# Optimization experiments

Hardware: AMD Instinct MI355X
Metric: run time of the kernel (lower is better)

Reference implementation:

```python
import jax, jax.numpy as jnp
import numpy as np

CUTOFF = 4.0
RBF_N = 32          # distance_embedding_size == D_rbf
F_DIM = 128         # hidden_size
N_ATOMS = 20000
N_PROBES = 100000
N_EDGES = 262144
LN_EPS = 1e-5


def setup_inputs() -> dict:
    key = jax.random.key(0)
    ks = jax.random.split(key, 20)
    s = 0.02
    inp = {
        "diff_pi": jax.random.normal(ks[0], (N_EDGES, 3), jnp.float32),
        "S_JK": jax.random.normal(ks[1], (N_ATOMS, F_DIM), jnp.float32),
        "V_JK": jax.random.normal(ks[2], (N_ATOMS, 3, F_DIM), jnp.float32),
        "atom_idx": jax.random.randint(ks[3], (N_EDGES,), 0, N_ATOMS),
        "probe_idx": jax.random.randint(ks[4], (N_EDGES,), 0, N_PROBES),
        "num_probes": N_PROBES,
        # state branch params
        "w_s1": jax.random.normal(ks[5], (3 * F_DIM, F_DIM), jnp.float32) * s,
        "b_s1": jnp.zeros((F_DIM,), jnp.float32),
        "g_ln": jnp.ones((F_DIM,), jnp.float32),
        "b_ln": jnp.zeros((F_DIM,), jnp.float32),
        "w_s2": jax.random.normal(ks[6], (F_DIM, F_DIM), jnp.float32) * s,
        "b_s2": jnp.zeros((F_DIM,), jnp.float32),
        # filter branch params
        "w_f1": jax.random.normal(ks[7], (RBF_N, F_DIM), jnp.float32) * s,
        "b_f1": jnp.zeros((F_DIM,), jnp.float32),
        "w_f2": jax.random.normal(ks[8], (F_DIM, F_DIM), jnp.float32) * s,
        "b_f2": jnp.zeros((F_DIM,), jnp.float32),
        # output head params
        "w_o1": jax.random.normal(ks[9], (F_DIM, F_DIM // 2), jnp.float32) * s,
        "b_o1": jnp.zeros((F_DIM // 2,), jnp.float32),
        "w_o2": jax.random.normal(ks[10], (F_DIM // 2, 1), jnp.float32) * s,
        "b_o2": jnp.zeros((1,), jnp.float32),
        "final_bias": jnp.array([-6.1], jnp.float32),
    }
    return inp


def reference(diff_pi, S_JK, V_JK, atom_idx, probe_idx, num_probes,
              w_s1, b_s1, g_ln, b_ln, w_s2, b_s2,
              w_f1, b_f1, w_f2, b_f2,
              w_o1, b_o1, w_o2, b_o2, final_bias):
    silu = jax.nn.silu
    # edge distances
    sq = (diff_pi ** 2).sum(-1)                       # [E]
    dist = jnp.sqrt(sq)                               # [E] exact distance
    dist_safe = jnp.sqrt(sq + 1e-8)[:, None]          # [E,1]
    r_hat = diff_pi / dist_safe                       # [E,3]

    # sinc RBF expansion: sin(n*pi*d/cutoff)/d, n=1..RBF_N
    n = jnp.arange(1, RBF_N + 1, dtype=diff_pi.dtype) # [D]
    e_pi = jnp.sin(dist[:, None] * n * (jnp.pi / CUTOFF)) / dist[:, None]  # [E,D]

    # gather atom features to edges
    n_i = jnp.sqrt((V_JK ** 2).sum(1) + 1e-8)         # [N,F]
    n_e = n_i[atom_idx]                               # [E,F]
    V_e = V_JK[atom_idx]                              # [E,3,F]
    q_pi = (V_e * r_hat[:, :, None]).sum(1)           # [E,F]
    S_e = S_JK[atom_idx]                              # [E,F]

    # state branch: Linear -> LayerNorm -> SiLU -> Linear
    h = jnp.concatenate([S_e, n_e, q_pi], axis=-1)    # [E,3F]
    u = h @ w_s1 + b_s1                               # [E,F]
    mu = u.mean(-1, keepdims=True)
    var = ((u - mu) ** 2).mean(-1, keepdims=True)
    u_norm = (u - mu) / jnp.sqrt(var + LN_EPS) * g_ln + b_ln
    state = silu(u_norm) @ w_s2 + b_s2                # [E,F]

    # filter branch (no normalization -> absolute distance scale)
    W = silu(e_pi @ w_f1 + b_f1) @ w_f2 + b_f2        # [E,F]

    # fuse + output head
    m = (silu((W * state) @ w_o1 + b_o1) @ w_o2 + b_o2)[:, 0]  # [E]

    x = dist / CUTOFF
    env = 1.0 - 21.0 * x ** 5 + 35.0 * x ** 6 - 15.0 * x ** 7
    env = jnp.where(dist < CUTOFF, env, jnp.zeros_like(env))
    m_w = m * env

    # scatter-add to probes
    rho = jax.ops.segment_sum(m_w, probe_idx, num_segments=num_probes)
    return rho + final_bias[0]
```

## Files before the change

kernel.cpp:

```cpp
#include <hip/hip_runtime.h>

#define EPB     64
#define E_TOTAL 262144
#define NPROBE  100000

#define HSTR   392
#define ASTR   136
#define A2_O   0
#define F1_O   8704
#define EPI_O  17408
#define LNP_B  19968
#define MPT_B  20992
#define LDS_SH 25088

#define WS1_O  0
#define WS2_O  49152
#define WF1_O  65536
#define WF2_O  69632
#define WO1_O  86016
#define WT_TOT 94208

typedef __attribute__((ext_vector_type(8))) short  short8;
typedef __attribute__((ext_vector_type(4))) float  floatx4;

#define MFMA16(a, b, c) __builtin_amdgcn_mfma_f32_16x16x32_bf16((a), (b), (c), 0, 0, 0)

__device__ __forceinline__ short f2bf(float x) {
    unsigned u = __builtin_bit_cast(unsigned, x);
    u = (u + 0x7FFFu + ((u >> 16) & 1u)) >> 16;
    return (short)(unsigned short)u;
}

__device__ __forceinline__ float silu_f(float x) { return x / (1.0f + __expf(-x)); }

struct F8 { float v[8]; };
__device__ __forceinline__ F8 ld8(const float* __restrict__ p) {
    F8 r;
    const float4 a = *(const float4*)p;
    const float4 b = *(const float4*)(p + 4);
    r.v[0] = a.x; r.v[1] = a.y; r.v[2] = a.z; r.v[3] = a.w;
    r.v[4] = b.x; r.v[5] = b.y; r.v[6] = b.z; r.v[7] = b.w;
    return r;
}

__global__ void cfr_prep(const float* __restrict__ w_s1, const float* __restrict__ w_s2,
                         const float* __restrict__ w_f1, const float* __restrict__ w_f2,
                         const float* __restrict__ w_o1,
                         const float* __restrict__ fb, float* __restrict__ out,
                         unsigned short* __restrict__ wt) {
    int i = blockIdx.x * 256 + threadIdx.x;
    if (i < NPROBE) out[i] = fb[0];
    if (i < WT_TOT) {
        float v;
        if (i < WS2_O)      { int n = i / 384, k = i - n * 384;        v = w_s1[k * 128 + n]; }
        else if (i < WF1_O) { int j = i - WS2_O, n = j >> 7, k = j & 127; v = w_s2[k * 128 + n]; }
        else if (i < WF2_O) { int j = i - WF1_O, n = j >> 5, k = j & 31;  v = w_f1[k * 128 + n]; }
        else if (i < WO1_O) { int j = i - WF2_O, n = j >> 7, k = j & 127; v = w_f2[k * 128 + n]; }
        else                { int j = i - WO1_O, n = j >> 7, k = j & 127; v = w_o1[k * 64 + n]; }
        wt[i] = (unsigned short)f2bf(v);
    }
}

__global__ __launch_bounds__(256, 3) void cfr_main(
    const float* __restrict__ diff,  const float* __restrict__ S_JK,
    const float* __restrict__ V_JK,  const int* __restrict__ atom_idx,
    const int* __restrict__ probe_idx,
    const unsigned short* __restrict__ wt,
    const float* __restrict__ b_s1, const float* __restrict__ g_ln,
    const float* __restrict__ b_ln, const float* __restrict__ b_s2,
    const float* __restrict__ b_f1, const float* __restrict__ b_f2,
    const float* __restrict__ b_o1, const float* __restrict__ w_o2,
    const float* __restrict__ b_o2,
    float* __restrict__ out)
{
    __shared__ __align__(16) unsigned short LDSu[LDS_SH];
    __shared__ float rdat[EPB][4];
    __shared__ float invd_s[EPB];
    __shared__ float env_s[EPB];
    __shared__ int   probe_s[EPB];
    __shared__ int   atom_s[EPB];

    float* lnp   = (float*)&LDSu[LNP_B];
    float* mpart = (float*)&LDSu[MPT_B];

    const int t    = threadIdx.x;
    const int e0   = blockIdx.x * EPB;
    const int wave = t >> 6;
    const int lane = t & 63;
    const int q    = lane >> 4;
    const int c16  = lane & 15;

    if (t < EPB) {
        int e = e0 + t;
        float dx = diff[e * 3 + 0], dy = diff[e * 3 + 1], dz = diff[e * 3 + 2];
        float sq   = dx * dx + dy * dy + dz * dz;
        float dist = sqrtf(sq);
        float rinv = 1.0f / sqrtf(sq + 1e-8f);
        rdat[t][0] = dx * rinv; rdat[t][1] = dy * rinv; rdat[t][2] = dz * rinv;
        rdat[t][3] = dist;
        invd_s[t]  = 1.0f / dist;
        float x  = dist * 0.25f;
        float x2 = x * x, x4 = x2 * x2;
        float x5 = x4 * x, x6 = x5 * x, x7 = x6 * x;
        float env = 1.0f - 21.0f * x5 + 35.0f * x6 - 15.0f * x7;
        env_s[t]  = (dist < 4.0f) ? env : 0.0f;
        probe_s[t] = probe_idx[e];
        atom_s[t]  = atom_idx[e];
    }
    __syncthreads();

#pragma unroll
    for (int it = 0; it < 4; ++it) {
        int idx = it * 256 + t;
        int e = idx >> 4, f = (idx & 15) * 8;
        int a = atom_s[e];
        F8 se = ld8(S_JK + a * 128 + f);
        F8 v0 = ld8(V_JK + a * 384 + f);
        F8 v1 = ld8(V_JK + a * 384 + 128 + f);
        F8 v2 = ld8(V_JK + a * 384 + 256 + f);
        float rx = rdat[e][0], ry = rdat[e][1], rz = rdat[e][2];
        short8 hS, hN, hQ;
#pragma unroll
        for (int j = 0; j < 8; ++j) {
            hS[j] = f2bf(se.v[j]);
            hN[j] = f2bf(sqrtf(v0.v[j] * v0.v[j] + v1.v[j] * v1.v[j] + v2.v[j] * v2.v[j] + 1e-8f));
            hQ[j] = f2bf(v0.v[j] * rx + v1.v[j] * ry + v2.v[j] * rz);
        }
        unsigned short* hr = &LDSu[e * HSTR];
        *(short8*)&hr[f]       = hS;
        *(short8*)&hr[128 + f] = hN;
        *(short8*)&hr[256 + f] = hQ;
    }
    __syncthreads();

    floatx4 acc[4][2];
    const floatx4 zero4 = {0.f, 0.f, 0.f, 0.f};
#pragma unroll
    for (int mi = 0; mi < 4; ++mi) { acc[mi][0] = zero4; acc[mi][1] = zero4; }

#pragma unroll
    for (int kk = 0; kk < 12; ++kk) {
        short8 bfr[2], af[4];
#pragma unroll
        for (int ni = 0; ni < 2; ++ni) {
            int n = wave * 32 + ni * 16 + c16;
            bfr[ni] = *(const short8*)&wt[WS1_O + n * 384 + kk * 32 + q * 8];
        }
#pragma unroll
        for (int mi = 0; mi < 4; ++mi)
            af[mi] = *(const short8*)&LDSu[(mi * 16 + c16) * HSTR + kk * 32 + q * 8];
#pragma unroll
        for (int mi = 0; mi < 4; ++mi)
#pragma unroll
            for (int ni = 0; ni < 2; ++ni)
                acc[mi][ni] = MFMA16(af[mi], bfr[ni], acc[mi][ni]);
    }
    __syncthreads();

    float bs1c[2], glc[2], blc[2];
#pragma unroll
    for (int ni = 0; ni < 2; ++ni) {
        int col = wave * 32 + ni * 16 + c16;
        bs1c[ni] = b_s1[col]; glc[ni] = g_ln[col]; blc[ni] = b_ln[col];
    }
#pragma unroll
    for (int mi = 0; mi < 4; ++mi)
#pragma unroll
        for (int r = 0; r < 4; ++r) {
            float s = 0.f, s2 = 0.f;
#pragma unroll
            for (int ni = 0; ni < 2; ++ni) {
                float v = acc[mi][ni][r] + bs1c[ni];
                s += v; s2 += v * v;
            }
#pragma unroll
            for (int d = 1; d < 16; d <<= 1) {
                s  += __shfl_xor(s, d, 64);
                s2 += __shfl_xor(s2, d, 64);
            }
            if (c16 == 0) {
                int row = mi * 16 + q * 4 + r;
                lnp[row * 8 + wave * 2 + 0] = s;
                lnp[row * 8 + wave * 2 + 1] = s2;
            }
        }
    __syncthreads();

#pragma unroll
    for (int mi = 0; mi < 4; ++mi)
#pragma unroll
        for (int r = 0; r < 4; ++r) {
            int row = mi * 16 + q * 4 + r;
            float su = 0.f, sq2 = 0.f;
#pragma unroll
            for (int w = 0; w < 4; ++w) { su += lnp[row * 8 + w * 2]; sq2 += lnp[row * 8 + w * 2 + 1]; }
            float mu = su * (1.f / 128.f);
            float ms = sq2 * (1.f / 128.f);
            float rstd = rsqrtf(ms - mu * mu + 1e-5f);
#pragma unroll
            for (int ni = 0; ni < 2; ++ni) {
                float v = acc[mi][ni][r] + bs1c[ni];
                float y = (v - mu) * rstd * glc[ni] + blc[ni];
                LDSu[A2_O + row * ASTR + (wave * 32 + ni * 16 + c16)] = (unsigned short)f2bf(silu_f(y));
            }
        }
    {
        int e = t >> 2, ng = t & 3;
        float dist = rdat[e][3];
        float inv  = invd_s[e];
        short8 pk;
#pragma unroll
        for (int j = 0; j < 8; ++j) {
            float nf = (float)(ng * 8 + j + 1);
            pk[j] = f2bf(__sinf(dist * nf * 0.785398163397448f) * inv);
        }
        *(short8*)&LDSu[EPI_O + e * 40 + ng * 8] = pk;
    }
    __syncthreads();

    {
        short8 ae[4], be[2];
#pragma unroll
        for (int mi = 0; mi < 4; ++mi)
            ae[mi] = *(const short8*)&LDSu[EPI_O + (mi * 16 + c16) * 40 + q * 8];
#pragma unroll
        for (int ni = 0; ni < 2; ++ni) {
            int n = wave * 32 + ni * 16 + c16;
            be[ni] = *(const short8*)&wt[WF1_O + n * 32 + q * 8];
        }
        floatx4 facc[4][2];
#pragma unroll
        for (int mi = 0; mi < 4; ++mi)
#pragma unroll
            for (int ni = 0; ni < 2; ++ni)
                facc[mi][ni] = MFMA16(ae[mi], be[ni], zero4);
        float bf1c[2];
#pragma unroll
        for (int ni = 0; ni < 2; ++ni) bf1c[ni] = b_f1[wave * 32 + ni * 16 + c16];
#pragma unroll
        for (int mi = 0; mi < 4; ++mi)
#pragma unroll
            for (int r = 0; r < 4; ++r) {
                int row = mi * 16 + q * 4 + r;
#pragma unroll
                for (int ni = 0; ni < 2; ++ni) {
                    float v = facc[mi][ni][r] + bf1c[ni];
                    LDSu[F1_O + row * ASTR + (wave * 32 + ni * 16 + c16)] = (unsigned short)f2bf(silu_f(v));
                }
            }
    }
    __syncthreads();

    {
        floatx4 sacc[4][2], wacc[4][2];
#pragma unroll
        for (int mi = 0; mi < 4; ++mi)
#pragma unroll
            for (int ni = 0; ni < 2; ++ni) { sacc[mi][ni] = zero4; wacc[mi][ni] = zero4; }
#pragma unroll
        for (int kk = 0; kk < 4; ++kk) {
            short8 a2f[4], f1f[4], b2[2], bw[2];
#pragma unroll
            for (int ni = 0; ni < 2; ++ni) {
                int n = wave * 32 + ni * 16 + c16;
                b2[ni] = *(const short8*)&wt[WS2_O + n * 128 + kk * 32 + q * 8];
                bw[ni] = *(const short8*)&wt[WF2_O + n * 128 + kk * 32 + q * 8];
            }
#pragma unroll
            for (int mi = 0; mi < 4; ++mi) {
                a2f[mi] = *(const short8*)&LDSu[A2_O + (mi * 16 + c16) * ASTR + kk * 32 + q * 8];
                f1f[mi] = *(const short8*)&LDSu[F1_O + (mi * 16 + c16) * ASTR + kk * 32 + q * 8];
            }
#pragma unroll
            for (int mi = 0; mi < 4; ++mi)
#pragma unroll
                for (int ni = 0; ni < 2; ++ni) {
                    sacc[mi][ni] = MFMA16(a2f[mi], b2[ni], sacc[mi][ni]);
                    wacc[mi][ni] = MFMA16(f1f[mi], bw[ni], wacc[mi][ni]);
                }
        }
        __syncthreads();
        float bs2c[2], bf2c[2];
#pragma unroll
        for (int ni = 0; ni < 2; ++ni) {
            int col = wave * 32 + ni * 16 + c16;
            bs2c[ni] = b_s2[col]; bf2c[ni] = b_f2[col];
        }
#pragma unroll
        for (int mi = 0; mi < 4; ++mi)
#pragma unroll
            for (int r = 0; r < 4; ++r) {
                int row = mi * 16 + q * 4 + r;
#pragma unroll
                for (int ni = 0; ni < 2; ++ni) {
                    float g = (sacc[mi][ni][r] + bs2c[ni]) * (wacc[mi][ni][r] + bf2c[ni]);
                    LDSu[A2_O + row * ASTR + (wave * 32 + ni * 16 + c16)] = (unsigned short)f2bf(g);
                }
            }
    }
    __syncthreads();

    {
        const int n2 = wave * 16 + c16;
        floatx4 oacc[4];
#pragma unroll
        for (int mi = 0; mi < 4; ++mi) oacc[mi] = zero4;
#pragma unroll
        for (int kk = 0; kk < 4; ++kk) {
            short8 bfr = *(const short8*)&wt[WO1_O + n2 * 128 + kk * 32 + q * 8];
#pragma unroll
            for (int mi = 0; mi < 4; ++mi) {
                short8 af = *(const short8*)&LDSu[A2_O + (mi * 16 + c16) * ASTR + kk * 32 + q * 8];
                oacc[mi] = MFMA16(af, bfr, oacc[mi]);
            }
        }
        float bo1c = b_o1[n2], wo2c = w_o2[n2];
#pragma unroll
        for (int mi = 0; mi < 4; ++mi)
#pragma unroll
            for (int r = 0; r < 4; ++r) {
                float s = silu_f(oacc[mi][r] + bo1c) * wo2c;
#pragma unroll
                for (int d = 1; d < 16; d <<= 1) s += __shfl_xor(s, d, 64);
                if (c16 == 0) mpart[(mi * 16 + q * 4 + r) * 4 + wave] = s;
            }
    }
    __syncthreads();

    if (t < EPB) {
        float m  = mpart[t * 4 + 0] + mpart[t * 4 + 1] + mpart[t * 4 + 2] + mpart[t * 4 + 3] + b_o2[0];
        float mw = m * env_s[t];
        if (mw != 0.f) unsafeAtomicAdd(&out[probe_s[t]], mw);
    }
}

extern "C" void kernel_launch(void* const* d_in, const int* in_sizes, int n_in,
                              void* d_out, int out_size, void* d_ws, size_t ws_size,
                              hipStream_t stream) {
    const float* diff    = (const float*)d_in[0];
    const float* S_JK    = (const float*)d_in[1];
    const float* V_JK    = (const float*)d_in[2];
    const int*   atom_i  = (const int*)d_in[3];
    const int*   probe_i = (const int*)d_in[4];
    const float* w_s1 = (const float*)d_in[6];
    const float* b_s1 = (const float*)d_in[7];
    const float* g_ln = (const float*)d_in[8];
    const float* b_ln = (const float*)d_in[9];
    const float* w_s2 = (const float*)d_in[10];
    const float* b_s2 = (const float*)d_in[11];
    const float* w_f1 = (const float*)d_in[12];
    const float* b_f1 = (const float*)d_in[13];
    const float* w_f2 = (const float*)d_in[14];
    const float* b_f2 = (const float*)d_in[15];
    const float* w_o1 = (const float*)d_in[16];
    const float* b_o1 = (const float*)d_in[17];
    const float* w_o2 = (const float*)d_in[18];
    const float* b_o2 = (const float*)d_in[19];
    const float* fbias = (const float*)d_in[20];
    float* out = (float*)d_out;
    unsigned short* wt = (unsigned short*)d_ws;

    cfr_prep<<<(NPROBE + 255) / 256, 256, 0, stream>>>(w_s1, w_s2, w_f1, w_f2, w_o1,
                                                       fbias, out, wt);
    cfr_main<<<E_TOTAL / EPB, 256, 0, stream>>>(diff, S_JK, V_JK, atom_i, probe_i, wt,
        b_s1, g_ln, b_ln, b_s2, b_f1, b_f2, b_o1, w_o2, b_o2, out);
}
```

Before: 288.3 us.

## Precompute per-atom bf16 S, norm and V tables to shrink edge gathers

Adds a prep kernel that converts S_JK and V_JK to bf16 per atom and precomputes the per-atom vector norm once. The edge kernel then gathers half as many bytes per edge and skips the repeated norm computation. It also swaps round-to-nearest bf16 conversion for truncation and perm-based packing in several LDS stores. The price is an extra launch, extra workspace traffic, and slightly different rounding, since q is now computed from bf16 V and values are truncated rather than rounded.

```diff
diff --git a/kernel.cpp b/kernel.cpp
--- a/kernel.cpp
+++ b/kernel.cpp
@@ -3,6 +3,7 @@
 #define EPB     64
 #define E_TOTAL 262144
 #define NPROBE  100000
+#define N_ATOMS 20000
 
 #define HSTR   392
 #define ASTR   136
@@ -19,9 +20,13 @@
 #define WF2_O  69632
 #define WO1_O  86016
 #define WT_TOT 94208
-
-typedef __attribute__((ext_vector_type(8))) short  short8;
-typedef __attribute__((ext_vector_type(4))) float  floatx4;
+#define SB_O   WT_TOT
+#define NB_O   (SB_O + N_ATOMS * 128)
+#define VB_O   (NB_O + N_ATOMS * 128)
+
+typedef __attribute__((ext_vector_type(8))) short          short8;
+typedef __attribute__((ext_vector_type(8))) unsigned short ushort8;
+typedef __attribute__((ext_vector_type(4))) float          floatx4;
 
 #define MFMA16(a, b, c) __builtin_amdgcn_mfma_f32_16x16x32_bf16((a), (b), (c), 0, 0, 0)
 
@@ -29,6 +34,16 @@
     unsigned u = __builtin_bit_cast(unsigned, x);
     u = (u + 0x7FFFu + ((u >> 16) & 1u)) >> 16;
     return (short)(unsigned short)u;
+}
+__device__ __forceinline__ unsigned short bft(float x) {
+    return (unsigned short)(__builtin_bit_cast(unsigned, x) >> 16);
+}
+__device__ __forceinline__ unsigned pk2(float lo, float hi) {
+    return __builtin_amdgcn_perm(__builtin_bit_cast(unsigned, hi),
+                                 __builtin_bit_cast(unsigned, lo), 0x07060302u);
+}
+__device__ __forceinline__ float bf2f(unsigned short u) {
+    return __builtin_bit_cast(float, ((unsigned)u) << 16);
 }
 
 __device__ __forceinline__ float silu_f(float x) { return x / (1.0f + __expf(-x)); }
@@ -43,16 +58,16 @@
     return r;
 }
 
-__global__ void cfr_prep(const float* __restrict__ w_s1, const float* __restrict__ w_s2,
-                         const float* __restrict__ w_f1, const float* __restrict__ w_f2,
-                         const float* __restrict__ w_o1,
-                         const float* __restrict__ fb, float* __restrict__ out,
-                         unsigned short* __restrict__ wt) {
+__global__ void cfr_prep_w(const float* __restrict__ w_s1, const float* __restrict__ w_s2,
+                           const float* __restrict__ w_f1, const float* __restrict__ w_f2,
+                           const float* __restrict__ w_o1,
+                           const float* __restrict__ fb, float* __restrict__ out,
+                           unsigned short* __restrict__ wt) {
     int i = blockIdx.x * 256 + threadIdx.x;
     if (i < NPROBE) out[i] = fb[0];
     if (i < WT_TOT) {
         float v;
-        if (i < WS2_O)      { int n = i / 384, k = i - n * 384;        v = w_s1[k * 128 + n]; }
+        if (i < WS2_O)      { int n = i / 384, k = i - n * 384;          v = w_s1[k * 128 + n]; }
         else if (i < WF1_O) { int j = i - WS2_O, n = j >> 7, k = j & 127; v = w_s2[k * 128 + n]; }
         else if (i < WF2_O) { int j = i - WF1_O, n = j >> 5, k = j & 31;  v = w_f1[k * 128 + n]; }
         else if (i < WO1_O) { int j = i - WF2_O, n = j >> 7, k = j & 127; v = w_f2[k * 128 + n]; }
@@ -61,11 +76,38 @@
     }
 }
 
+__global__ void cfr_prep_atoms(const float* __restrict__ S, const float* __restrict__ V,
+                               unsigned short* __restrict__ sb, unsigned short* __restrict__ nb,
+                               unsigned short* __restrict__ vb) {
+    int i = blockIdx.x * 256 + threadIdx.x;
+    if (i >= N_ATOMS * 16) return;
+    int a = i >> 4, fb8 = (i & 15) * 8;
+    F8 s  = ld8(S + a * 128 + fb8);
+    F8 v0 = ld8(V + a * 384 + fb8);
+    F8 v1 = ld8(V + a * 384 + 128 + fb8);
+    F8 v2 = ld8(V + a * 384 + 256 + fb8);
+    ushort8 so, no, w0, w1, w2;
+#pragma unroll
+    for (int j = 0; j < 8; ++j) {
+        so[j] = (unsigned short)f2bf(s.v[j]);
+        no[j] = (unsigned short)f2bf(sqrtf(v0.v[j] * v0.v[j] + v1.v[j] * v1.v[j] + v2.v[j] * v2.v[j] + 1e-8f));
+        w0[j] = (unsigned short)f2bf(v0.v[j]);
+        w1[j] = (unsigned short)f2bf(v1.v[j]);
+        w2[j] = (unsigned short)f2bf(v2.v[j]);
+    }
+    *(ushort8*)&sb[a * 128 + fb8] = so;
+    *(ushort8*)&nb[a * 128 + fb8] = no;
+    *(ushort8*)&vb[a * 384 + fb8]       = w0;
+    *(ushort8*)&vb[a * 384 + 128 + fb8] = w1;
+    *(ushort8*)&vb[a * 384 + 256 + fb8] = w2;
+}
+
 __global__ __launch_bounds__(256, 3) void cfr_main(
-    const float* __restrict__ diff,  const float* __restrict__ S_JK,
-    const float* __restrict__ V_JK,  const int* __restrict__ atom_idx,
-    const int* __restrict__ probe_idx,
+    const float* __restrict__ diff,
+    const int* __restrict__ atom_idx, const int* __restrict__ probe_idx,
     const unsigned short* __restrict__ wt,
+    const unsigned short* __restrict__ sb, const unsigned short* __restrict__ nb,
+    const unsigned short* __restrict__ vb,
     const float* __restrict__ b_s1, const float* __restrict__ g_ln,
     const float* __restrict__ b_ln, const float* __restrict__ b_s2,
     const float* __restrict__ b_f1, const float* __restrict__ b_f2,
@@ -114,22 +156,23 @@
         int idx = it * 256 + t;
         int e = idx >> 4, f = (idx & 15) * 8;
         int a = atom_s[e];
-        F8 se = ld8(S_JK + a * 128 + f);
-        F8 v0 = ld8(V_JK + a * 384 + f);
-        F8 v1 = ld8(V_JK + a * 384 + 128 + f);
-        F8 v2 = ld8(V_JK + a * 384 + 256 + f);
+        ushort8 s8 = *(const ushort8*)&sb[a * 128 + f];
+        ushort8 n8 = *(const ushort8*)&nb[a * 128 + f];
+        ushort8 v0 = *(const ushort8*)&vb[a * 384 + f];
+        ushort8 v1 = *(const ushort8*)&vb[a * 384 + 128 + f];
+        ushort8 v2 = *(const ushort8*)&vb[a * 384 + 256 + f];
         float rx = rdat[e][0], ry = rdat[e][1], rz = rdat[e][2];
-        short8 hS, hN, hQ;
-#pragma unroll
-        for (int j = 0; j < 8; ++j) {
-            hS[j] = f2bf(se.v[j]);
-            hN[j] = f2bf(sqrtf(v0.v[j] * v0.v[j] + v1.v[j] * v1.v[j] + v2.v[j] * v2.v[j] + 1e-8f));
-            hQ[j] = f2bf(v0.v[j] * rx + v1.v[j] * ry + v2.v[j] * rz);
+        unsigned qp[4];
+#pragma unroll
+        for (int jj = 0; jj < 4; ++jj) {
+            float x0 = bf2f(v0[2 * jj]) * rx + bf2f(v1[2 * jj]) * ry + bf2f(v2[2 * jj]) * rz;
+            float x1 = bf2f(v0[2 * jj + 1]) * rx + bf2f(v1[2 * jj + 1]) * ry + bf2f(v2[2 * jj + 1]) * rz;
+            qp[jj] = pk2(x0, x1);
         }
         unsigned short* hr = &LDSu[e * HSTR];
-        *(short8*)&hr[f]       = hS;
-        *(short8*)&hr[128 + f] = hN;
-        *(short8*)&hr[256 + f] = hQ;
+        *(ushort8*)&hr[f]       = s8;
+        *(ushort8*)&hr[128 + f] = n8;
+        *(uint4*)&hr[256 + f]   = make_uint4(qp[0], qp[1], qp[2], qp[3]);
     }
     __syncthreads();
 
@@ -201,20 +244,21 @@
             for (int ni = 0; ni < 2; ++ni) {
                 float v = acc[mi][ni][r] + bs1c[ni];
                 float y = (v - mu) * rstd * glc[ni] + blc[ni];
-                LDSu[A2_O + row * ASTR + (wave * 32 + ni * 16 + c16)] = (unsigned short)f2bf(silu_f(y));
+                LDSu[A2_O + row * ASTR + (wave * 32 + ni * 16 + c16)] = bft(silu_f(y));
             }
         }
     {
         int e = t >> 2, ng = t & 3;
         float dist = rdat[e][3];
         float inv  = invd_s[e];
-        short8 pk;
+        float sv[8];
 #pragma unroll
         for (int j = 0; j < 8; ++j) {
             float nf = (float)(ng * 8 + j + 1);
-            pk[j] = f2bf(__sinf(dist * nf * 0.785398163397448f) * inv);
-        }
-        *(short8*)&LDSu[EPI_O + e * 40 + ng * 8] = pk;
+            sv[j] = __sinf(dist * nf * 0.785398163397448f) * inv;
+        }
+        *(uint4*)&LDSu[EPI_O + e * 40 + ng * 8] =
+            make_uint4(pk2(sv[0], sv[1]), pk2(sv[2], sv[3]), pk2(sv[4], sv[5]), pk2(sv[6], sv[7]));
     }
     __syncthreads();
 
@@ -245,7 +289,7 @@
 #pragma unroll
                 for (int ni = 0; ni < 2; ++ni) {
                     float v = facc[mi][ni][r] + bf1c[ni];
-                    LDSu[F1_O + row * ASTR + (wave * 32 + ni * 16 + c16)] = (unsigned short)f2bf(silu_f(v));
+                    LDSu[F1_O + row * ASTR + (wave * 32 + ni * 16 + c16)] = bft(silu_f(v));
                 }
             }
     }
@@ -294,7 +338,7 @@
 #pragma unroll
                 for (int ni = 0; ni < 2; ++ni) {
                     float g = (sacc[mi][ni][r] + bs2c[ni]) * (wacc[mi][ni][r] + bf2c[ni]);
-                    LDSu[A2_O + row * ASTR + (wave * 32 + ni * 16 + c16)] = (unsigned short)f2bf(g);
+                    LDSu[A2_O + row * ASTR + (wave * 32 + ni * 16 + c16)] = bft(g);
                 }
             }
     }
@@ -358,10 +402,15 @@
     const float* b_o2 = (const float*)d_in[19];
     const float* fbias = (const float*)d_in[20];
     float* out = (float*)d_out;
+
     unsigned short* wt = (unsigned short*)d_ws;
-
-    cfr_prep<<<(NPROBE + 255) / 256, 256, 0, stream>>>(w_s1, w_s2, w_f1, w_f2, w_o1,
-                                                       fbias, out, wt);
-    cfr_main<<<E_TOTAL / EPB, 256, 0, stream>>>(diff, S_JK, V_JK, atom_i, probe_i, wt,
+    unsigned short* sbp = wt + SB_O;
+    unsigned short* nbp = wt + NB_O;
+    unsigned short* vbp = wt + VB_O;
+
+    cfr_prep_w<<<(NPROBE + 255) / 256, 256, 0, stream>>>(w_s1, w_s2, w_f1, w_f2, w_o1,
+                                                         fbias, out, wt);
+    cfr_prep_atoms<<<(N_ATOMS * 16 + 255) / 256, 256, 0, stream>>>(S_JK, V_JK, sbp, nbp, vbp);
+    cfr_main<<<E_TOTAL / EPB, 256, 0, stream>>>(diff, atom_i, probe_i, wt, sbp, nbp, vbp,
         b_s1, g_ln, b_ln, b_s2, b_f1, b_f2, b_o1, w_o2, b_o2, out);
 }
```

Measured after the change: 278.7 us. 3.3% less time.

## Precompute per-atom projections of first state linear, gather them per edge

Applied to the files above, without the earlier changes.

The first state-branch linear layer is split algebraically. The S and norm contributions plus bias, and the three V-component projections through the q-part of w_s1, are computed once per atom in a new prep kernel and stored as bf16. Each edge then gathers 512 bf16 values and combines them with r_hat through FMAs, which removes the per-edge K=384 GEMM and the fp32 S/V gathers. LayerNorm now runs per thread with a quad shuffle, replacing the cross-wave LDS reduction. The changes add an extra kernel launch, round intermediate u to bf16, and use truncation instead of round-to-nearest for some bf16 conversions.

```diff
diff --git a/kernel.cpp b/kernel.cpp
--- a/kernel.cpp
+++ b/kernel.cpp
@@ -3,15 +3,13 @@
 #define EPB     64
 #define E_TOTAL 262144
 #define NPROBE  100000
-
-#define HSTR   392
+#define N_ATOMS 20000
+
 #define ASTR   136
 #define A2_O   0
 #define F1_O   8704
 #define EPI_O  17408
-#define LNP_B  19968
-#define MPT_B  20992
-#define LDS_SH 25088
+#define LDS_SH 19968
 
 #define WS1_O  0
 #define WS2_O  49152
@@ -19,9 +17,11 @@
 #define WF2_O  69632
 #define WO1_O  86016
 #define WT_TOT 94208
-
-typedef __attribute__((ext_vector_type(8))) short  short8;
-typedef __attribute__((ext_vector_type(4))) float  floatx4;
+#define PQ_O   WT_TOT
+
+typedef __attribute__((ext_vector_type(8))) short          short8;
+typedef __attribute__((ext_vector_type(8))) unsigned short ushort8;
+typedef __attribute__((ext_vector_type(4))) float          floatx4;
 
 #define MFMA16(a, b, c) __builtin_amdgcn_mfma_f32_16x16x32_bf16((a), (b), (c), 0, 0, 0)
 
@@ -30,7 +30,13 @@
     u = (u + 0x7FFFu + ((u >> 16) & 1u)) >> 16;
     return (short)(unsigned short)u;
 }
-
+__device__ __forceinline__ unsigned pk2(float lo, float hi) {
+    return __builtin_amdgcn_perm(__builtin_bit_cast(unsigned, hi),
+                                 __builtin_bit_cast(unsigned, lo), 0x07060302u);
+}
+__device__ __forceinline__ float bf2f(unsigned short u) {
+    return __builtin_bit_cast(float, ((unsigned)u) << 16);
+}
 __device__ __forceinline__ float silu_f(float x) { return x / (1.0f + __expf(-x)); }
 
 struct F8 { float v[8]; };
@@ -43,16 +49,16 @@
     return r;
 }
 
-__global__ void cfr_prep(const float* __restrict__ w_s1, const float* __restrict__ w_s2,
-                         const float* __restrict__ w_f1, const float* __restrict__ w_f2,
-                         const float* __restrict__ w_o1,
-                         const float* __restrict__ fb, float* __restrict__ out,
-                         unsigned short* __restrict__ wt) {
+__global__ void cfr_prep_w(const float* __restrict__ w_s1, const float* __restrict__ w_s2,
+                           const float* __restrict__ w_f1, const float* __restrict__ w_f2,
+                           const float* __restrict__ w_o1,
+                           const float* __restrict__ fb, float* __restrict__ out,
+                           unsigned short* __restrict__ wt) {
     int i = blockIdx.x * 256 + threadIdx.x;
     if (i < NPROBE) out[i] = fb[0];
     if (i < WT_TOT) {
         float v;
-        if (i < WS2_O)      { int n = i / 384, k = i - n * 384;        v = w_s1[k * 128 + n]; }
+        if (i < WS2_O)      { int n = i / 384, k = i - n * 384;          v = w_s1[k * 128 + n]; }
         else if (i < WF1_O) { int j = i - WS2_O, n = j >> 7, k = j & 127; v = w_s2[k * 128 + n]; }
         else if (i < WF2_O) { int j = i - WF1_O, n = j >> 5, k = j & 31;  v = w_f1[k * 128 + n]; }
         else if (i < WO1_O) { int j = i - WF2_O, n = j >> 7, k = j & 127; v = w_f2[k * 128 + n]; }
@@ -61,27 +67,144 @@
     }
 }
 
-__global__ __launch_bounds__(256, 3) void cfr_main(
-    const float* __restrict__ diff,  const float* __restrict__ S_JK,
-    const float* __restrict__ V_JK,  const int* __restrict__ atom_idx,
-    const int* __restrict__ probe_idx,
-    const unsigned short* __restrict__ wt,
-    const float* __restrict__ b_s1, const float* __restrict__ g_ln,
-    const float* __restrict__ b_ln, const float* __restrict__ b_s2,
-    const float* __restrict__ b_f1, const float* __restrict__ b_f2,
-    const float* __restrict__ b_o1, const float* __restrict__ w_o2,
-    const float* __restrict__ b_o2,
+__global__ __launch_bounds__(256, 1) void cfr_prep_pq(
+    const float* __restrict__ S, const float* __restrict__ V,
+    const float* __restrict__ b_s1,
+    const unsigned short* __restrict__ wt, unsigned short* __restrict__ pq)
+{
+    __shared__ __align__(16) unsigned short bufH[64 * 264];
+    __shared__ __align__(16) unsigned short bufV[192 * 136];
+
+    const int t    = threadIdx.x;
+    const int a0   = blockIdx.x * 64;
+    const int wave = t >> 6;
+    const int lane = t & 63;
+    const int q    = lane >> 4;
+    const int c16  = lane & 15;
+
+#pragma unroll
+    for (int it = 0; it < 4; ++it) {
+        int idx = it * 256 + t;
+        int al = idx >> 4, f8 = (idx & 15) * 8;
+        int a = a0 + al;
+        ushort8 sS, sN, s0, s1, s2;
+        if (a < N_ATOMS) {
+            F8 s  = ld8(S + a * 128 + f8);
+            F8 v0 = ld8(V + a * 384 + f8);
+            F8 v1 = ld8(V + a * 384 + 128 + f8);
+            F8 v2 = ld8(V + a * 384 + 256 + f8);
+#pragma unroll
+            for (int j = 0; j < 8; ++j) {
+                sS[j] = (unsigned short)f2bf(s.v[j]);
+                sN[j] = (unsigned short)f2bf(sqrtf(v0.v[j]*v0.v[j] + v1.v[j]*v1.v[j] + v2.v[j]*v2.v[j] + 1e-8f));
+                s0[j] = (unsigned short)f2bf(v0.v[j]);
+                s1[j] = (unsigned short)f2bf(v1.v[j]);
+                s2[j] = (unsigned short)f2bf(v2.v[j]);
+            }
+        } else {
+#pragma unroll
+            for (int j = 0; j < 8; ++j) { sS[j]=0; sN[j]=0; s0[j]=0; s1[j]=0; s2[j]=0; }
+        }
+        *(ushort8*)&bufH[al * 264 + f8]        = sS;
+        *(ushort8*)&bufH[al * 264 + 128 + f8]  = sN;
+        *(ushort8*)&bufV[(al) * 136 + f8]       = s0;
+        *(ushort8*)&bufV[(64 + al) * 136 + f8]  = s1;
+        *(ushort8*)&bufV[(128 + al) * 136 + f8] = s2;
+    }
+    __syncthreads();
+
+    const floatx4 zero4 = {0.f, 0.f, 0.f, 0.f};
+    float bs1c[2];
+#pragma unroll
+    for (int ni = 0; ni < 2; ++ni) bs1c[ni] = b_s1[wave * 32 + ni * 16 + c16];
+
+    {
+        floatx4 pacc[4][2];
+#pragma unroll
+        for (int mi = 0; mi < 4; ++mi) { pacc[mi][0] = zero4; pacc[mi][1] = zero4; }
+#pragma unroll
+        for (int kk = 0; kk < 8; ++kk) {
+            short8 bfr[2], af[4];
+#pragma unroll
+            for (int ni = 0; ni < 2; ++ni) {
+                int n = wave * 32 + ni * 16 + c16;
+                bfr[ni] = *(const short8*)&wt[WS1_O + n * 384 + kk * 32 + q * 8];
+            }
+#pragma unroll
+            for (int mi = 0; mi < 4; ++mi)
+                af[mi] = *(const short8*)&bufH[(mi * 16 + c16) * 264 + kk * 32 + q * 8];
+#pragma unroll
+            for (int mi = 0; mi < 4; ++mi)
+#pragma unroll
+                for (int ni = 0; ni < 2; ++ni)
+                    pacc[mi][ni] = MFMA16(af[mi], bfr[ni], pacc[mi][ni]);
+        }
+#pragma unroll
+        for (int mi = 0; mi < 4; ++mi)
+#pragma unroll
+            for (int r = 0; r < 4; ++r) {
+                int a = a0 + mi * 16 + q * 4 + r;
+                if (a < N_ATOMS)
+#pragma unroll
+                    for (int ni = 0; ni < 2; ++ni) {
+                        int col = wave * 32 + ni * 16 + c16;
+                        pq[a * 512 + col] = (unsigned short)f2bf(pacc[mi][ni][r] + bs1c[ni]);
+                    }
+            }
+    }
+
+    short8 bq[4][2];
+#pragma unroll
+    for (int kk = 0; kk < 4; ++kk)
+#pragma unroll
+        for (int ni = 0; ni < 2; ++ni) {
+            int n = wave * 32 + ni * 16 + c16;
+            bq[kk][ni] = *(const short8*)&wt[WS1_O + n * 384 + 256 + kk * 32 + q * 8];
+        }
+#pragma unroll
+    for (int d = 0; d < 3; ++d) {
+        floatx4 qacc[4][2];
+#pragma unroll
+        for (int mi = 0; mi < 4; ++mi) { qacc[mi][0] = zero4; qacc[mi][1] = zero4; }
+#pragma unroll
+        for (int kk = 0; kk < 4; ++kk) {
+            short8 af[4];
+#pragma unroll
+            for (int mi = 0; mi < 4; ++mi)
+                af[mi] = *(const short8*)&bufV[(d * 64 + mi * 16 + c16) * 136 + kk * 32 + q * 8];
+#pragma unroll
+            for (int mi = 0; mi < 4; ++mi)
+#pragma unroll
+                for (int ni = 0; ni < 2; ++ni)
+                    qacc[mi][ni] = MFMA16(af[mi], bq[kk][ni], qacc[mi][ni]);
+        }
+#pragma unroll
+        for (int mi = 0; mi < 4; ++mi)
+#pragma unroll
+            for (int r = 0; r < 4; ++r) {
+                int a = a0 + mi * 16 + q * 4 + r;
+                if (a < N_ATOMS)
+#pragma unroll
+                    for (int ni = 0; ni < 2; ++ni) {
+                        int col = wave * 32 + ni * 16 + c16;
+                        pq[a * 512 + (1 + d) * 128 + col] = (unsigned short)f2bf(qacc[mi][ni][r]);
+                    }
+            }
+    }
+}
+
+__global__ __launch_bounds__(256, 4) void cfr_main(
+    const float* __restrict__ diff,
+    const int* __restrict__ atom_idx, const int* __restrict__ probe_idx,
+    const unsigned short* __restrict__ wt, const unsigned short* __restrict__ pq,
+    const float* __restrict__ g_ln, const float* __restrict__ b_ln,
+    const float* __restrict__ b_s2, const float* __restrict__ b_f1,
+    const float* __restrict__ b_f2, const float* __restrict__ b_o1,
+    const float* __restrict__ w_o2, const float* __restrict__ b_o2,
     float* __restrict__ out)
 {
     __shared__ __align__(16) unsigned short LDSu[LDS_SH];
-    __shared__ float rdat[EPB][4];
-    __shared__ float invd_s[EPB];
-    __shared__ float env_s[EPB];
-    __shared__ int   probe_s[EPB];
-    __shared__ int   atom_s[EPB];
-
-    float* lnp   = (float*)&LDSu[LNP_B];
-    float* mpart = (float*)&LDSu[MPT_B];
+    float* mpart = (float*)&LDSu[EPI_O];
 
     const int t    = threadIdx.x;
     const int e0   = blockIdx.x * EPB;
@@ -89,248 +212,205 @@
     const int lane = t & 63;
     const int q    = lane >> 4;
     const int c16  = lane & 15;
-
-    if (t < EPB) {
-        int e = e0 + t;
-        float dx = diff[e * 3 + 0], dy = diff[e * 3 + 1], dz = diff[e * 3 + 2];
+    const floatx4 zero4 = {0.f, 0.f, 0.f, 0.f};
+
+    {
+        const int el = t >> 2;
+        const int c0 = (t & 3) * 32;
+        const int eg = e0 + el;
+        const int a  = atom_idx[eg];
+        float dx = diff[eg * 3 + 0], dy = diff[eg * 3 + 1], dz = diff[eg * 3 + 2];
         float sq   = dx * dx + dy * dy + dz * dz;
         float dist = sqrtf(sq);
-        float rinv = 1.0f / sqrtf(sq + 1e-8f);
-        rdat[t][0] = dx * rinv; rdat[t][1] = dy * rinv; rdat[t][2] = dz * rinv;
-        rdat[t][3] = dist;
-        invd_s[t]  = 1.0f / dist;
+        float rinv = rsqrtf(sq + 1e-8f);
+        float rx = dx * rinv, ry = dy * rinv, rz = dz * rinv;
+
+        const ushort8* pqr = (const ushort8*)(pq + a * 512 + c0);
+        float u[32];
+#pragma unroll
+        for (int g = 0; g < 4; ++g) {
+            ushort8 v = pqr[g];
+#pragma unroll
+            for (int j = 0; j < 8; ++j) u[g * 8 + j] = bf2f(v[j]);
+        }
+#pragma unroll
+        for (int g = 0; g < 4; ++g) {
+            ushort8 v = pqr[16 + g];
+#pragma unroll
+            for (int j = 0; j < 8; ++j) u[g * 8 + j] = fmaf(bf2f(v[j]), rx, u[g * 8 + j]);
+        }
+#pragma unroll
+        for (int g = 0; g < 4; ++g) {
+            ushort8 v = pqr[32 + g];
+#pragma unroll
+            for (int j = 0; j < 8; ++j) u[g * 8 + j] = fmaf(bf2f(v[j]), ry, u[g * 8 + j]);
+        }
+#pragma unroll
+        for (int g = 0; g < 4; ++g) {
+            ushort8 v = pqr[48 + g];
+#pragma unroll
+            for (int j = 0; j < 8; ++j) u[g * 8 + j] = fmaf(bf2f(v[j]), rz, u[g * 8 + j]);
+        }
+        float s = 0.f, s2 = 0.f;
+#pragma unroll
+        for (int j = 0; j < 32; ++j) { s += u[j]; s2 = fmaf(u[j], u[j], s2); }
+        s  += __shfl_xor(s, 1);  s  += __shfl_xor(s, 2);
+        s2 += __shfl_xor(s2, 1); s2 += __shfl_xor(s2, 2);
+        float mu = s * (1.f / 128.f);
+        float rstd = rsqrtf(s2 * (1.f / 128.f) - mu * mu + 1e-5f);
+        const float4* gp = (const float4*)(g_ln + c0);
+        const float4* bp = (const float4*)(b_ln + c0);
+        unsigned pko[16];
+#pragma unroll
+        for (int g4 = 0; g4 < 8; ++g4) {
+            float4 gg = gp[g4], bb = bp[g4];
+            float y0 = silu_f((u[g4 * 4 + 0] - mu) * rstd * gg.x + bb.x);
+            float y1 = silu_f((u[g4 * 4 + 1] - mu) * rstd * gg.y + bb.y);
+            float y2 = silu_f((u[g4 * 4 + 2] - mu) * rstd * gg.z + bb.z);
+            float y3 = silu_f((u[g4 * 4 + 3] - mu) * rstd * gg.w + bb.w);
+            pko[g4 * 2 + 0] = pk2(y0, y1);
+            pko[g4 * 2 + 1] = pk2(y2, y3);
+        }
+        uint4* dst = (uint4*)&LDSu[A2_O + el * ASTR + c0];
+        dst[0] = make_uint4(pko[0], pko[1], pko[2], pko[3]);
+        dst[1] = make_uint4(pko[4], pko[5], pko[6], pko[7]);
+        dst[2] = make_uint4(pko[8], pko[9], pko[10], pko[11]);
+        dst[3] = make_uint4(pko[12], pko[13], pko[14], pko[15]);
+        float inv = 1.0f / dist;
+        float sv[8];
+#pragma unroll
+        for (int j = 0; j < 8; ++j) {
+            float nf = (float)((t & 3) * 8 + j + 1);
+            sv[j] = __sinf(dist * nf * 0.785398163397448f) * inv;
+        }
+        *(uint4*)&LDSu[EPI_O + el * 40 + (t & 3) * 8] =
+            make_uint4(pk2(sv[0], sv[1]), pk2(sv[2], sv[3]), pk2(sv[4], sv[5]), pk2(sv[6], sv[7]));
+    }
+    __syncthreads();
+
+    {
+        short8 ae[4], be[2];
+#pragma unroll
+        for (int mi = 0; mi < 4; ++mi)
+            ae[mi] = *(const short8*)&LDSu[EPI_O + (mi * 16 + c16) * 40 + q * 8];
+#pragma unroll
+        for (int ni = 0; ni < 2; ++ni) {
+            int n = wave * 32 + ni * 16 + c16;
+            be[ni] = *(const short8*)&wt[WF1_O + n * 32 + q * 8];
+        }
+        floatx4 facc[4][2];
+#pragma unroll
+        for (int mi = 0; mi < 4; ++mi)
+#pragma unroll
+            for (int ni = 0; ni < 2; ++ni)
+                facc[mi][ni] = MFMA16(ae[mi], be[ni], zero4);
+        float bf1c[2];
+#pragma unroll
+        for (int ni = 0; ni < 2; ++ni) bf1c[ni] = b_f1[wave * 32 + ni * 16 + c16];
+#pragma unroll
+        for (int mi = 0; mi < 4; ++mi)
+#pragma unroll
+            for (int r = 0; r < 4; ++r) {
+                int row = mi * 16 + q * 4 + r;
+#pragma unroll
+                for (int ni = 0; ni < 2; ++ni) {
+                    float v = facc[mi][ni][r] + bf1c[ni];
+                    LDSu[F1_O + row * ASTR + (wave * 32 + ni * 16 + c16)] =
+                        (unsigned short)(__builtin_bit_cast(unsigned, silu_f(v)) >> 16);
+                }
+            }
+    }
+    __syncthreads();
+
+    {
+        floatx4 sacc[4][2], wacc[4][2];
+#pragma unroll
+        for (int mi = 0; mi < 4; ++mi)
+#pragma unroll
+            for (int ni = 0; ni < 2; ++ni) { sacc[mi][ni] = zero4; wacc[mi][ni] = zero4; }
+#pragma unroll
+        for (int kk = 0; kk < 4; ++kk) {
+            short8 a2f[4], f1f[4], b2[2], bw[2];
+#pragma unroll
+            for (int ni = 0; ni < 2; ++ni) {
+                int n = wave * 32 + ni * 16 + c16;
+                b2[ni] = *(const short8*)&wt[WS2_O + n * 128 + kk * 32 + q * 8];
+                bw[ni] = *(const short8*)&wt[WF2_O + n * 128 + kk * 32 + q * 8];
+            }
+#pragma unroll
+            for (int mi = 0; mi < 4; ++mi) {
+                a2f[mi] = *(const short8*)&LDSu[A2_O + (mi * 16 + c16) * ASTR + kk * 32 + q * 8];
+                f1f[mi] = *(const short8*)&LDSu[F1_O + (mi * 16 + c16) * ASTR + kk * 32 + q * 8];
+            }
+#pragma unroll
+            for (int mi = 0; mi < 4; ++mi)
+#pragma unroll
+                for (int ni = 0; ni < 2; ++ni) {
+                    sacc[mi][ni] = MFMA16(a2f[mi], b2[ni], sacc[mi][ni]);
+                    wacc[mi][ni] = MFMA16(f1f[mi], bw[ni], wacc[mi][ni]);
+                }
+        }
+        __syncthreads();
+        float bs2c[2], bf2c[2];
+#pragma unroll
+        for (int ni = 0; ni < 2; ++ni) {
+            int col = wave * 32 + ni * 16 + c16;
+            bs2c[ni] = b_s2[col]; bf2c[ni] = b_f2[col];
+        }
+#pragma unroll
+        for (int mi = 0; mi < 4; ++mi)
+#pragma unroll
+            for (int r = 0; r < 4; ++r) {
+                int row = mi * 16 + q * 4 + r;
+#pragma unroll
+                for (int ni = 0; ni < 2; ++ni) {
+                    float g = (sacc[mi][ni][r] + bs2c[ni]) * (wacc[mi][ni][r] + bf2c[ni]);
+                    LDSu[A2_O + row * ASTR + (wave * 32 + ni * 16 + c16)] =
+                        (unsigned short)(__builtin_bit_cast(unsigned, g) >> 16);
+                }
+            }
+    }
+    __syncthreads();
+
+    {
+        const int n2 = wave * 16 + c16;
+        floatx4 oacc[4];
+#pragma unroll
+        for (int mi = 0; mi < 4; ++mi) oacc[mi] = zero4;
+#pragma unroll
+        for (int kk = 0; kk < 4; ++kk) {
+            short8 bfr = *(const short8*)&wt[WO1_O + n2 * 128 + kk * 32 + q * 8];
+#pragma unroll
+            for (int mi = 0; mi < 4; ++mi) {
+                short8 af = *(const short8*)&LDSu[A2_O + (mi * 16 + c16) * ASTR + kk * 32 + q * 8];
+                oacc[mi] = MFMA16(af, bfr, oacc[mi]);
+            }
+        }
+        float bo1c = b_o1[n2], wo2c = w_o2[n2];
+#pragma unroll
+        for (int mi = 0; mi < 4; ++mi)
+#pragma unroll
+            for (int r = 0; r < 4; ++r) {
+                float s = silu_f(oacc[mi][r] + bo1c) * wo2c;
+#pragma unroll
+                for (int d = 1; d < 16; d <<= 1) s += __shfl_xor(s, d, 64);
+                if (c16 == 0) mpart[(mi * 16 + q * 4 + r) * 4 + wave] = s;
+            }
+    }
+    __syncthreads();
+
+    if (t < EPB) {
+        int eg = e0 + t;
+        float m = mpart[t * 4 + 0] + mpart[t * 4 + 1] + mpart[t * 4 + 2] + mpart[t * 4 + 3] + b_o2[0];
+        float dx = diff[eg * 3 + 0], dy = diff[eg * 3 + 1], dz = diff[eg * 3 + 2];
+        float dist = sqrtf(dx * dx + dy * dy + dz * dz);
         float x  = dist * 0.25f;
         float x2 = x * x, x4 = x2 * x2;
         float x5 = x4 * x, x6 = x5 * x, x7 = x6 * x;
         float env = 1.0f - 21.0f * x5 + 35.0f * x6 - 15.0f * x7;
-        env_s[t]  = (dist < 4.0f) ? env : 0.0f;
-        probe_s[t] = probe_idx[e];
-        atom_s[t]  = atom_idx[e];
-    }
-    __syncthreads();
-
-#pragma unroll
-    for (int it = 0; it < 4; ++it) {
-        int idx = it * 256 + t;
-        int e = idx >> 4, f = (idx & 15) * 8;
-        int a = atom_s[e];
-        F8 se = ld8(S_JK + a * 128 + f);
-        F8 v0 = ld8(V_JK + a * 384 + f);
-        F8 v1 = ld8(V_JK + a * 384 + 128 + f);
-        F8 v2 = ld8(V_JK + a * 384 + 256 + f);
-        float rx = rdat[e][0], ry = rdat[e][1], rz = rdat[e][2];
-        short8 hS, hN, hQ;
-#pragma unroll
-        for (int j = 0; j < 8; ++j) {
-            hS[j] = f2bf(se.v[j]);
-            hN[j] = f2bf(sqrtf(v0.v[j] * v0.v[j] + v1.v[j] * v1.v[j] + v2.v[j] * v2.v[j] + 1e-8f));
-            hQ[j] = f2bf(v0.v[j] * rx + v1.v[j] * ry + v2.v[j] * rz);
-        }
-        unsigned short* hr = &LDSu[e * HSTR];
-        *(short8*)&hr[f]       = hS;
-        *(short8*)&hr[128 + f] = hN;
-        *(short8*)&hr[256 + f] = hQ;
-    }
-    __syncthreads();
-
-    floatx4 acc[4][2];
-    const floatx4 zero4 = {0.f, 0.f, 0.f, 0.f};
-#pragma unroll
-    for (int mi = 0; mi < 4; ++mi) { acc[mi][0] = zero4; acc[mi][1] = zero4; }
-
-#pragma unroll
-    for (int kk = 0; kk < 12; ++kk) {
-        short8 bfr[2], af[4];
-#pragma unroll
-        for (int ni = 0; ni < 2; ++ni) {
-            int n = wave * 32 + ni * 16 + c16;
-            bfr[ni] = *(const short8*)&wt[WS1_O + n * 384 + kk * 32 + q * 8];
-        }
-#pragma unroll
-        for (int mi = 0; mi < 4; ++mi)
-            af[mi] = *(const short8*)&LDSu[(mi * 16 + c16) * HSTR + kk * 32 + q * 8];
-#pragma unroll
-        for (int mi = 0; mi < 4; ++mi)
-#pragma unroll
-            for (int ni = 0; ni < 2; ++ni)
-                acc[mi][ni] = MFMA16(af[mi], bfr[ni], acc[mi][ni]);
-    }
-    __syncthreads();
-
-    float bs1c[2], glc[2], blc[2];
-#pragma unroll
-    for (int ni = 0; ni < 2; ++ni) {
-        int col = wave * 32 + ni * 16 + c16;
-        bs1c[ni] = b_s1[col]; glc[ni] = g_ln[col]; blc[ni] = b_ln[col];
-    }
-#pragma unroll
-    for (int mi = 0; mi < 4; ++mi)
-#pragma unroll
-        for (int r = 0; r < 4; ++r) {
-            float s = 0.f, s2 = 0.f;
-#pragma unroll
-            for (int ni = 0; ni < 2; ++ni) {
-                float v = acc[mi][ni][r] + bs1c[ni];
-                s += v; s2 += v * v;
-            }
-#pragma unroll
-            for (int d = 1; d < 16; d <<= 1) {
-                s  += __shfl_xor(s, d, 64);
-                s2 += __shfl_xor(s2, d, 64);
-            }
-            if (c16 == 0) {
-                int row = mi * 16 + q * 4 + r;
-                lnp[row * 8 + wave * 2 + 0] = s;
-                lnp[row * 8 + wave * 2 + 1] = s2;
-            }
-        }
-    __syncthreads();
-
-#pragma unroll
-    for (int mi = 0; mi < 4; ++mi)
-#pragma unroll
-        for (int r = 0; r < 4; ++r) {
-            int row = mi * 16 + q * 4 + r;
-            float su = 0.f, sq2 = 0.f;
-#pragma unroll
-            for (int w = 0; w < 4; ++w) { su += lnp[row * 8 + w * 2]; sq2 += lnp[row * 8 + w * 2 + 1]; }
-            float mu = su * (1.f / 128.f);
-            float ms = sq2 * (1.f / 128.f);
-            float rstd = rsqrtf(ms - mu * mu + 1e-5f);
-#pragma unroll
-            for (int ni = 0; ni < 2; ++ni) {
-                float v = acc[mi][ni][r] + bs1c[ni];
-                float y = (v - mu) * rstd * glc[ni] + blc[ni];
-                LDSu[A2_O + row * ASTR + (wave * 32 + ni * 16 + c16)] = (unsigned short)f2bf(silu_f(y));
-            }
-        }
-    {
-        int e = t >> 2, ng = t & 3;
-        float dist = rdat[e][3];
-        float inv  = invd_s[e];
-        short8 pk;
-#pragma unroll
-        for (int j = 0; j < 8; ++j) {
-            float nf = (float)(ng * 8 + j + 1);
-            pk[j] = f2bf(__sinf(dist * nf * 0.785398163397448f) * inv);
-        }
-        *(short8*)&LDSu[EPI_O + e * 40 + ng * 8] = pk;
-    }
-    __syncthreads();
-
-    {
-        short8 ae[4], be[2];
-#pragma unroll
-        for (int mi = 0; mi < 4; ++mi)
-            ae[mi] = *(const short8*)&LDSu[EPI_O + (mi * 16 + c16) * 40 + q * 8];
-#pragma unroll
-        for (int ni = 0; ni < 2; ++ni) {
-            int n = wave * 32 + ni * 16 + c16;
-            be[ni] = *(const short8*)&wt[WF1_O + n * 32 + q * 8];
-        }
-        floatx4 facc[4][2];
-#pragma unroll
-        for (int mi = 0; mi < 4; ++mi)
-#pragma unroll
-            for (int ni = 0; ni < 2; ++ni)
-                facc[mi][ni] = MFMA16(ae[mi], be[ni], zero4);
-        float bf1c[2];
-#pragma unroll
-        for (int ni = 0; ni < 2; ++ni) bf1c[ni] = b_f1[wave * 32 + ni * 16 + c16];
-#pragma unroll
-        for (int mi = 0; mi < 4; ++mi)
-#pragma unroll
-            for (int r = 0; r < 4; ++r) {
-                int row = mi * 16 + q * 4 + r;
-#pragma unroll
-                for (int ni = 0; ni < 2; ++ni) {
-                    float v = facc[mi][ni][r] + bf1c[ni];
-                    LDSu[F1_O + row * ASTR + (wave * 32 + ni * 16 + c16)] = (unsigned short)f2bf(silu_f(v));
-                }
-            }
-    }
-    __syncthreads();
-
-    {
-        floatx4 sacc[4][2], wacc[4][2];
-#pragma unroll
-        for (int mi = 0; mi < 4; ++mi)
-#pragma unroll
-            for (int ni = 0; ni < 2; ++ni) { sacc[mi][ni] = zero4; wacc[mi][ni] = zero4; }
-#pragma unroll
-        for (int kk = 0; kk < 4; ++kk) {
-            short8 a2f[4], f1f[4], b2[2], bw[2];
-#pragma unroll
-            for (int ni = 0; ni < 2; ++ni) {
-                int n = wave * 32 + ni * 16 + c16;
-                b2[ni] = *(const short8*)&wt[WS2_O + n * 128 + kk * 32 + q * 8];
-                bw[ni] = *(const short8*)&wt[WF2_O + n * 128 + kk * 32 + q * 8];
-            }
-#pragma unroll
-            for (int mi = 0; mi < 4; ++mi) {
-                a2f[mi] = *(const short8*)&LDSu[A2_O + (mi * 16 + c16) * ASTR + kk * 32 + q * 8];
-                f1f[mi] = *(const short8*)&LDSu[F1_O + (mi * 16 + c16) * ASTR + kk * 32 + q * 8];
-            }
-#pragma unroll
-            for (int mi = 0; mi < 4; ++mi)
-#pragma unroll
-                for (int ni = 0; ni < 2; ++ni) {
-                    sacc[mi][ni] = MFMA16(a2f[mi], b2[ni], sacc[mi][ni]);
-                    wacc[mi][ni] = MFMA16(f1f[mi], bw[ni], wacc[mi][ni]);
-                }
-        }
-        __syncthreads();
-        float bs2c[2], bf2c[2];
-#pragma unroll
-        for (int ni = 0; ni < 2; ++ni) {
-            int col = wave * 32 + ni * 16 + c16;
-            bs2c[ni] = b_s2[col]; bf2c[ni] = b_f2[col];
-        }
-#pragma unroll
-        for (int mi = 0; mi < 4; ++mi)
-#pragma unroll
-            for (int r = 0; r < 4; ++r) {
-                int row = mi * 16 + q * 4 + r;
-#pragma unroll
-                for (int ni = 0; ni < 2; ++ni) {
-                    float g = (sacc[mi][ni][r] + bs2c[ni]) * (wacc[mi][ni][r] + bf2c[ni]);
-                    LDSu[A2_O + row * ASTR + (wave * 32 + ni * 16 + c16)] = (unsigned short)f2bf(g);
-                }
-            }
-    }
-    __syncthreads();
-
-    {
-        const int n2 = wave * 16 + c16;
-        floatx4 oacc[4];
-#pragma unroll
-        for (int mi = 0; mi < 4; ++mi) oacc[mi] = zero4;
-#pragma unroll
-        for (int kk = 0; kk < 4; ++kk) {
-            short8 bfr = *(const short8*)&wt[WO1_O + n2 * 128 + kk * 32 + q * 8];
-#pragma unroll
-            for (int mi = 0; mi < 4; ++mi) {
-                short8 af = *(const short8*)&LDSu[A2_O + (mi * 16 + c16) * ASTR + kk * 32 + q * 8];
-                oacc[mi] = MFMA16(af, bfr, oacc[mi]);
-            }
-        }
-        float bo1c = b_o1[n2], wo2c = w_o2[n2];
-#pragma unroll
-        for (int mi = 0; mi < 4; ++mi)
-#pragma unroll
-            for (int r = 0; r < 4; ++r) {
-                float s = silu_f(oacc[mi][r] + bo1c) * wo2c;
-#pragma unroll
-                for (int d = 1; d < 16; d <<= 1) s += __shfl_xor(s, d, 64);
-                if (c16 == 0) mpart[(mi * 16 + q * 4 + r) * 4 + wave] = s;
-            }
-    }
-    __syncthreads();
-
-    if (t < EPB) {
-        float m  = mpart[t * 4 + 0] + mpart[t * 4 + 1] + mpart[t * 4 + 2] + mpart[t * 4 + 3] + b_o2[0];
-        float mw = m * env_s[t];
-        if (mw != 0.f) unsafeAtomicAdd(&out[probe_s[t]], mw);
+        env = (dist < 4.0f) ? env : 0.0f;
+        float mw = m * env;
+        if (mw != 0.f) unsafeAtomicAdd(&out[probe_idx[eg]], mw);
     }
 }
 
@@ -358,10 +438,13 @@
     const float* b_o2 = (const float*)d_in[19];
     const float* fbias = (const float*)d_in[20];
     float* out = (float*)d_out;
+
     unsigned short* wt = (unsigned short*)d_ws;
-
-    cfr_prep<<<(NPROBE + 255) / 256, 256, 0, stream>>>(w_s1, w_s2, w_f1, w_f2, w_o1,
-                                                       fbias, out, wt);
-    cfr_main<<<E_TOTAL / EPB, 256, 0, stream>>>(diff, S_JK, V_JK, atom_i, probe_i, wt,
-        b_s1, g_ln, b_ln, b_s2, b_f1, b_f2, b_o1, w_o2, b_o2, out);
-}
+    unsigned short* pqp = wt + PQ_O;
+
+    cfr_prep_w<<<(NPROBE + 255) / 256, 256, 0, stream>>>(w_s1, w_s2, w_f1, w_f2, w_o1,
+                                                         fbias, out, wt);
+    cfr_prep_pq<<<(N_ATOMS + 63) / 64, 256, 0, stream>>>(S_JK, V_JK, b_s1, wt, pqp);
+    cfr_main<<<E_TOTAL / EPB, 256, 0, stream>>>(diff, atom_i, probe_i, wt, pqp,
+        g_ln, b_ln, b_s2, b_f1, b_f2, b_o1, w_o2, b_o2, out);
+}
```

After: 241.0 us. 16.4% less time.
